# Optimization experiments

Hardware: AMD Instinct MI355X
Metric: run time of the kernel (lower is better)

Reference implementation:

```python
import jax, jax.numpy as jnp
import numpy as np

MODEL_DIM = 2048
NUM_HEADS = 32
HEAD_DIM = 64
NUM_KV_HEADS = 8
ROPE_BASE = 10000.0
BATCH = 2
SEQ = 2048


def setup_inputs() -> dict:
    key = jax.random.key(0)
    ks = jax.random.split(key, 5)
    sd = 1.0 / np.sqrt(MODEL_DIM)
    x = jax.random.normal(ks[0], (BATCH, SEQ, MODEL_DIM), dtype=jnp.float32)
    Wq = jax.random.normal(ks[1], (MODEL_DIM, NUM_HEADS * HEAD_DIM), dtype=jnp.float32) * sd
    Wk = jax.random.normal(ks[2], (MODEL_DIM, NUM_KV_HEADS * HEAD_DIM), dtype=jnp.float32) * sd
    Wv = jax.random.normal(ks[3], (MODEL_DIM, NUM_KV_HEADS * HEAD_DIM), dtype=jnp.float32) * sd
    Wo = jax.random.normal(ks[4], (NUM_HEADS * HEAD_DIM, MODEL_DIM), dtype=jnp.float32) * sd
    return {"x": x, "Wq": Wq, "Wk": Wk, "Wv": Wv, "Wo": Wo}


def _rope_cache(seq_len, head_dim, base, dtype):
    # inv_freq over even dims, standard rotate-half (Llama-style) RoPE cache
    inv_freq = 1.0 / (base ** (jnp.arange(0, head_dim, 2, dtype=jnp.float32) / head_dim))
    t = jnp.arange(seq_len, dtype=jnp.float32)
    freqs = jnp.outer(t, inv_freq)               # [S, hd/2]
    emb = jnp.concatenate([freqs, freqs], axis=-1)  # [S, hd]
    return jnp.cos(emb).astype(dtype), jnp.sin(emb).astype(dtype)


def _rotate_half(x):
    h = x.shape[-1] // 2
    return jnp.concatenate([-x[..., h:], x[..., :h]], axis=-1)


def _apply_rope(q, k, cos, sin):
    # q,k: [B, H, S, hd]; cos,sin: [S, hd] -> broadcast over batch/heads
    cos = cos[None, None, :, :]
    sin = sin[None, None, :, :]
    q = q * cos + _rotate_half(q) * sin
    k = k * cos + _rotate_half(k) * sin
    return q, k


def reference(x, Wq, Wk, Wv, Wo):
    bsz, seq_len, _ = x.shape
    q_per_kv = NUM_HEADS // NUM_KV_HEADS

    # projections -> [B, H, S, hd]
    q = (x @ Wq).reshape(bsz, seq_len, NUM_HEADS, HEAD_DIM).transpose(0, 2, 1, 3)
    k = (x @ Wk).reshape(bsz, seq_len, NUM_KV_HEADS, HEAD_DIM).transpose(0, 2, 1, 3)
    v = (x @ Wv).reshape(bsz, seq_len, NUM_KV_HEADS, HEAD_DIM).transpose(0, 2, 1, 3)

    # GQA: repeat_interleave KV heads to match Q heads
    k = jnp.repeat(k, q_per_kv, axis=1)
    v = jnp.repeat(v, q_per_kv, axis=1)

    cos, sin = _rope_cache(seq_len, HEAD_DIM, ROPE_BASE, x.dtype)
    q, k = _apply_rope(q, k, cos, sin)

    scale = 1.0 / np.sqrt(HEAD_DIM)
    scores = jnp.einsum('bhqd,bhkd->bhqk', q, k) * scale  # [B,H,S,S]
    causal = jnp.tril(jnp.ones((seq_len, seq_len), dtype=bool))
    scores = jnp.where(causal[None, None], scores, jnp.finfo(scores.dtype).min)
    attn = jax.nn.softmax(scores, axis=-1)
    y = jnp.einsum('bhqk,bhkd->bhqd', attn, v)  # [B,H,S,hd]

    y = y.transpose(0, 2, 1, 3).reshape(bsz, seq_len, NUM_HEADS * HEAD_DIM)
    return y @ Wo
```

## Files before the change

### kernel.cpp

```cpp
#include <hip/hip_runtime.h>
#include <cstdint>

typedef unsigned short u16;
typedef __attribute__((ext_vector_type(8))) short short8;
typedef __attribute__((ext_vector_type(4))) short short4v;
typedef __attribute__((ext_vector_type(4))) float f32x4;

#define SEQ     2048
#define NHEADS  32
#define NKV     8
#define HD      64
#define DM      2048
#define MROWS   4096
#define KVSTR   1024
#define PSTR    88

__device__ __forceinline__ float b2f(unsigned int u) {
    return __builtin_bit_cast(float, u << 16);
}
__device__ __forceinline__ u16 f2b(float f) {
    unsigned int u = __builtin_bit_cast(unsigned int, f);
    return (u16)((u + 0x7fffu + ((u >> 16) & 1u)) >> 16);
}
__device__ __forceinline__ unsigned int cvt_pk_bf16(float lo, float hi) {
    unsigned int r;
    asm("v_cvt_pk_bf16_f32 %0, %1, %2" : "=v"(r) : "v"(lo), "v"(hi));
    return r;
}
__device__ __forceinline__ float exp2_raw(float x) {
    return __builtin_amdgcn_exp2f(x);
}

__device__ __forceinline__ float dpp_red_max16(float x) {
    int v = __builtin_bit_cast(int, x);
    x = fmaxf(x, __builtin_bit_cast(float,
        __builtin_amdgcn_update_dpp(v, v, 0xB1, 0xF, 0xF, true)));
    v = __builtin_bit_cast(int, x);
    x = fmaxf(x, __builtin_bit_cast(float,
        __builtin_amdgcn_update_dpp(v, v, 0x4E, 0xF, 0xF, true)));
    v = __builtin_bit_cast(int, x);
    x = fmaxf(x, __builtin_bit_cast(float,
        __builtin_amdgcn_update_dpp(v, v, 0x141, 0xF, 0xF, true)));
    v = __builtin_bit_cast(int, x);
    x = fmaxf(x, __builtin_bit_cast(float,
        __builtin_amdgcn_update_dpp(v, v, 0x140, 0xF, 0xF, true)));
    return x;
}
__device__ __forceinline__ float dpp_red_sum16(float x) {
    int v = __builtin_bit_cast(int, x);
    x = x + __builtin_bit_cast(float,
        __builtin_amdgcn_update_dpp(v, v, 0xB1, 0xF, 0xF, true));
    v = __builtin_bit_cast(int, x);
    x = x + __builtin_bit_cast(float,
        __builtin_amdgcn_update_dpp(v, v, 0x4E, 0xF, 0xF, true));
    v = __builtin_bit_cast(int, x);
    x = x + __builtin_bit_cast(float,
        __builtin_amdgcn_update_dpp(v, v, 0x141, 0xF, 0xF, true));
    v = __builtin_bit_cast(int, x);
    x = x + __builtin_bit_cast(float,
        __builtin_amdgcn_update_dpp(v, v, 0x140, 0xF, 0xF, true));
    return x;
}

#define GLOAD_LDS16(g, l)                                              \
    __builtin_amdgcn_global_load_lds(                                  \
        (const __attribute__((address_space(1))) void*)(g),            \
        (__attribute__((address_space(3))) void*)(l), 16, 0, 0)

__global__ __launch_bounds__(256) void cvt_f32_bf16(
    const float* __restrict__ in, u16* __restrict__ out, int n4) {
    int i = blockIdx.x * 256 + threadIdx.x;
    if (i < n4) {
        float4 v = ((const float4*)in)[i];
        ushort4 o;
        o.x = f2b(v.x); o.y = f2b(v.y); o.z = f2b(v.z); o.w = f2b(v.w);
        ((ushort4*)out)[i] = o;
    }
}

__global__ __launch_bounds__(256) void rope_table_kernel(
    float* __restrict__ cosT, float* __restrict__ sinT) {
    int idx = blockIdx.x * 256 + threadIdx.x;
    int s  = idx >> 5;
    int dl = idx & 31;
    float inv_freq = exp2f((float)dl * -0.41524101186092025f);
    float ang = (float)s * inv_freq;
    float sn, cs;
    sincosf(ang, &sn, &cs);
    cosT[idx] = cs;
    sinT[idx] = sn;
}

__global__ __launch_bounds__(256) void transpose_f32_bf16(
    const float* __restrict__ in, u16* __restrict__ out, int K, int N) {
    __shared__ float tile[32][33];
    int n0 = blockIdx.x * 32, k0 = blockIdx.y * 32;
    int tx = threadIdx.x, ty = threadIdx.y;
    for (int r = ty; r < 32; r += 8)
        tile[r][tx] = in[(size_t)(k0 + r) * N + n0 + tx];
    __syncthreads();
    for (int r = ty; r < 32; r += 8)
        out[(size_t)(n0 + r) * K + k0 + tx] = f2b(tile[tx][r]);
}

#define GEMM_BODY(Aptr, BTptr, Kdim)                                        \
    __shared__ __align__(16) u16 rA[3][4096];                               \
    __shared__ __align__(16) u16 rB[3][4096];                               \
    const int tid  = threadIdx.x;                                           \
    const int wid  = tid >> 6;                                              \
    const int lane = tid & 63;                                              \
    const int quad = lane >> 4;                                             \
    const int l16  = lane & 15;                                             \
    const int nwg  = gridDim.x * gridDim.y;                                 \
    const int fid  = blockIdx.y * gridDim.x + blockIdx.x;                   \
    const int swz  = (fid & 7) * (nwg >> 3) + (fid >> 3);                   \
    const int rowBase = (swz / gridDim.x) * 128;                            \
    const int colBase = (swz % gridDim.x) * 128;                            \
    const int wr = (wid >> 1) * 64;                                         \
    const int wc = (wid & 1) * 64;                                          \
    size_t sAoff[2], sBoff[2];                                              \
    int ldOff[2];                                                           \
    _Pragma("unroll")                                                       \
    for (int j = 0; j < 2; ++j) {                                           \
        const int p = j * 256 + tid;       \
        const int q = p >> 3;                                               \
        const int u = (p & 7) ^ (q & 7);               \
        const int r = (q << 1) | (u >> 2);                                  \
        const int sc = (u & 3) * 8;              \
        sAoff[j] = (size_t)(rowBase + r) * (Kdim) + sc;                     \
        sBoff[j] = (size_t)(colBase + r) * (Kdim) + sc;                     \
        ldOff[j] = (j * 256 + (wid << 6)) * 8;    \
    }                                                                       \
    int aOff[4], bOff[4];                  \
    _Pragma("unroll")                                                       \
    for (int mi = 0; mi < 4; ++mi) {                                        \
        const int ra = wr + mi * 16 + l16;                                  \
        const int qa = ra >> 1;                                             \
        const int ua = ((ra & 1) << 2) | quad;                              \
        aOff[mi] = (qa * 8 + (ua ^ (qa & 7))) * 8;                          \
        const int rb = wc + mi * 16 + l16;                                  \
        const int qb = rb >> 1;                                             \
        const int ub = ((rb & 1) << 2) | quad;                              \
        bOff[mi] = (qb * 8 + (ub ^ (qb & 7))) * 8;                          \
    }                                                                       \
    f32x4 acc[4][4] = {};                                                   \
    const int NT = (Kdim) / 32;                                             \
    _Pragma("unroll")                                                       \
    for (int st = 0; st < 2; ++st) {         \
        _Pragma("unroll")                                                   \
        for (int j = 0; j < 2; ++j) {                                       \
            GLOAD_LDS16(Aptr  + sAoff[j] + st * 32, &rA[st][ldOff[j]]);     \
            GLOAD_LDS16(BTptr + sBoff[j] + st * 32, &rB[st][ldOff[j]]);     \
        }                                                                   \
    }                                                                       \
    int bs = 0;                            \
    for (int s = 0; s < NT; ++s) {                                          \
        if (s < NT - 1)                                                     \
            asm volatile("s_waitcnt vmcnt(4)\n\ts_barrier" ::: "memory");   \
        else                                                                \
            asm volatile("s_waitcnt vmcnt(0)\n\ts_barrier" ::: "memory");   \
        const u16* Ab = rA[bs];                                             \
        const u16* Bb = rB[bs];                                             \
        short8 a[4], b[4];                                                  \
        _Pragma("unroll")                                                   \
        for (int mi = 0; mi < 4; ++mi) a[mi] = *(const short8*)&Ab[aOff[mi]]; \
        _Pragma("unroll")                                                   \
        for (int ni = 0; ni < 4; ++ni) b[ni] = *(const short8*)&Bb[bOff[ni]]; \
        if (s + 2 < NT) {                    \
            const int bi = bs == 0 ? 2 : bs - 1;               \
            const int kk = (s + 2) * 32;                                    \
            _Pragma("unroll")                                               \
            for (int j = 0; j < 2; ++j) {                                   \
                GLOAD_LDS16(Aptr  + sAoff[j] + kk, &rA[bi][ldOff[j]]);      \
                GLOAD_LDS16(BTptr + sBoff[j] + kk, &rB[bi][ldOff[j]]);      \
            }                                                               \
        }                                                                   \
        __builtin_amdgcn_s_setprio(1);                                      \
        _Pragma("unroll")                                                   \
        for (int mi = 0; mi < 4; ++mi)                                      \
            _Pragma("unroll")                                               \
            for (int ni = 0; ni < 4; ++ni)                                  \
                acc[mi][ni] = __builtin_amdgcn_mfma_f32_16x16x32_bf16(      \
                    a[mi], b[ni], acc[mi][ni], 0, 0, 0);                    \
        __builtin_amdgcn_s_setprio(0);                                      \
        bs = bs == 2 ? 0 : bs + 1;                                          \
    }                                                                       \
    const int wRow = rowBase + wr;                                          \
    const int wCol = colBase + wc;

__global__ __launch_bounds__(256, 3) void gemm_qkv(
    const u16* __restrict__ A, const u16* __restrict__ BT,
    u16* __restrict__ Qb, u16* __restrict__ KVb,
    const float* __restrict__ cosT, const float* __restrict__ sinT) {
    GEMM_BODY(A, BT, DM)

    u16* dst;
    int dstride, dcol;
    float scale;
    bool doRope;
    if (wCol < 2048)      { dst = Qb;  dstride = 2048; dcol = wCol;
                            scale = 0.18033688011112042f; doRope = true;  }
    else if (wCol < 2560) { dst = KVb; dstride = 1024; dcol = wCol - 2048; scale = 1.0f; doRope = true;  }
    else                  { dst = KVb; dstride = 1024; dcol = wCol - 2048; scale = 1.0f; doRope = false; }

#pragma unroll
    for (int mi = 0; mi < 4; ++mi) {
#pragma unroll
        for (int r = 0; r < 4; ++r) {
            const int R = wRow + mi * 16 + quad * 4 + r;
            u16* crow = dst + (size_t)R * dstride + dcol;
            if (doRope) {
                const int s = R & (SEQ - 1);
#pragma unroll
                for (int ni = 0; ni < 2; ++ni) {
                    const int dl = ni * 16 + l16;
                    float lo = acc[mi][ni][r];
                    float hi = acc[mi][ni + 2][r];
                    float cs = cosT[s * 32 + dl];
                    float sn = sinT[s * 32 + dl];
                    crow[dl]      = f2b((lo * cs - hi * sn) * scale);
                    crow[dl + 32] = f2b((hi * cs + lo * sn) * scale);
                }
            } else {
#pragma unroll
                for (int ni = 0; ni < 4; ++ni)
                    crow[ni * 16 + l16] = f2b(acc[mi][ni][r]);
            }
        }
    }
}

__global__ __launch_bounds__(256, 3) void gemm_out(
    const u16* __restrict__ A, const u16* __restrict__ BT,
    float* __restrict__ C32) {
    GEMM_BODY(A, BT, DM)
#pragma unroll
    for (int mi = 0; mi < 4; ++mi) {
#pragma unroll
        for (int r = 0; r < 4; ++r) {
            const int R = wRow + mi * 16 + quad * 4 + r;
            float* crow = C32 + (size_t)R * DM + wCol;
#pragma unroll
            for (int ni = 0; ni < 4; ++ni)
                crow[ni * 16 + l16] = acc[mi][ni][r];
        }
    }
}

__global__ __launch_bounds__(256, 3) void flash_attn(
    const u16* __restrict__ Q, const u16* __restrict__ KV,
    u16* __restrict__ Yb, float* __restrict__ PoA,
    float* __restrict__ Ml) {
    __shared__ __align__(16) u16 Ks[64 * 64];
    __shared__ __align__(16) u16 Vt[64 * 72];
    __shared__ __align__(16) u16 Ps[4 * 32 * PSTR];

    const int p   = blockIdx.x >> 1;
    const int sh  = blockIdx.x & 1;
    const int h   = blockIdx.y;
    const int b   = blockIdx.z;
    const int kvh = h >> 2;
    const int tid  = threadIdx.x;
    const int wid  = tid >> 6;
    const int lane = tid & 63;
    const int quad = lane >> 4;
    const int l16  = lane & 15;

    const u16* Kg = KV + (size_t)b * SEQ * KVSTR + kvh * HD;
    const u16* Vg = Kg + 512;
    u16* Psw = Ps + wid * 32 * PSTR;

    const int kKey = tid >> 2;
    const int kC0  = (tid & 3) * 2;
    const int vkp  = tid & 31;
    const int vd0  = (tid >> 5) * 8;

    for (int ph = 0; ph < 2; ++ph) {
        const int qt = ph ? (15 - p) : p;
        const int hc = ph ? (16 - p) : (p + 1);
        const int tS = sh * hc;
        const int rowBaseW = qt * 128 + wid * 32;

        short8 qf[2][2];
#pragma unroll
        for (int rt = 0; rt < 2; ++rt)
#pragma unroll
            for (int ks = 0; ks < 2; ++ks)
                qf[rt][ks] = *(const short8*)&Q[
                    (size_t)(b * SEQ + rowBaseW + rt * 16 + l16) * (NHEADS * HD)
                    + h * HD + ks * 32 + quad * 8];

        f32x4 o[2][4] = {};
        float mi[8], li[8];
#pragma unroll
        for (int i = 0; i < 8; ++i) { mi[i] = -3e38f; li[i] = 0.f; }

        const size_t jF = (size_t)tS * 64;
        short8 kreg0 = *(const short8*)&Kg[(jF + kKey) * KVSTR + kC0 * 8];
        short8 kreg1 = *(const short8*)&Kg[(jF + kKey) * KVSTR + kC0 * 8 + 8];
        short8 vA = *(const short8*)&Vg[(jF + 2 * vkp)     * KVSTR + vd0];
        short8 vB = *(const short8*)&Vg[(jF + 2 * vkp + 1) * KVSTR + vd0];

        for (int tt = 0; tt < hc; ++tt) {
            const int j0 = (tS + tt) * 64;
            __syncthreads();

            *(short8*)&Ks[kKey * 64 + (((kC0)     ^ (kKey & 7)) * 8)] = kreg0;
            *(short8*)&Ks[kKey * 64 + (((kC0 + 1) ^ (kKey & 7)) * 8)] = kreg1;
#pragma unroll
            for (int i = 0; i < 8; ++i) {
                unsigned int w = (unsigned int)(u16)vA[i]
                               | ((unsigned int)(u16)vB[i] << 16);
                ((unsigned int*)Vt)[(vd0 + i) * 36 + vkp] = w;
            }
            __syncthreads();

            if (tt + 1 < hc) {
                const size_t jn = (size_t)(j0 + 64);
                kreg0 = *(const short8*)&Kg[(jn + kKey) * KVSTR + kC0 * 8];
                kreg1 = *(const short8*)&Kg[(jn + kKey) * KVSTR + kC0 * 8 + 8];
                vA = *(const short8*)&Vg[(jn + 2 * vkp)     * KVSTR + vd0];
                vB = *(const short8*)&Vg[(jn + 2 * vkp + 1) * KVSTR + vd0];
            }

            f32x4 s[2][4] = {};
#pragma unroll
            for (int ks = 0; ks < 2; ++ks)
#pragma unroll
                for (int ct = 0; ct < 4; ++ct) {
                    int key = ct * 16 + l16;
                    int cc  = (ks * 4 + quad) ^ (key & 7);
                    short8 bk = *(const short8*)&Ks[key * 64 + cc * 8];
                    s[0][ct] = __builtin_amdgcn_mfma_f32_16x16x32_bf16(
                        qf[0][ks], bk, s[0][ct], 0, 0, 0);
                    s[1][ct] = __builtin_amdgcn_mfma_f32_16x16x32_bf16(
                        qf[1][ks], bk, s[1][ct], 0, 0, 0);
                }

#pragma unroll
            for (int rt = 0; rt < 2; ++rt) {
                const int rB = rowBaseW + rt * 16;
                if (j0 + 63 > rB) {
#pragma unroll
                    for (int ct = 0; ct < 4; ++ct)
#pragma unroll
                        for (int r = 0; r < 4; ++r) {
                            int R = rB + quad * 4 + r;
                            int J = j0 + ct * 16 + l16;
                            if (J > R) s[rt][ct][r] = -3e38f;
                        }
                }
            }

#pragma unroll
            for (int rt = 0; rt < 2; ++rt)
#pragma unroll
                for (int r = 0; r < 4; ++r) {
                    const int ix = rt * 4 + r;
                    float rmax = fmaxf(fmaxf(s[rt][0][r], s[rt][1][r]),
                                       fmaxf(s[rt][2][r], s[rt][3][r]));
                    rmax = dpp_red_max16(rmax);
                    if (!__all(rmax <= mi[ix] + 11.54f)) {
                        float mnew  = fmaxf(mi[ix], rmax);
                        float alpha = exp2_raw(mi[ix] - mnew);
                        mi[ix] = mnew;
                        li[ix] *= alpha;
#pragma unroll
                        for (int ct = 0; ct < 4; ++ct) o[rt][ct][r] *= alpha;
                    }
                    float rs = 0.f;
#pragma unroll
                    for (int ct = 0; ct < 4; ++ct) {
                        float pv = exp2_raw(s[rt][ct][r] - mi[ix]);
                        s[rt][ct][r] = pv;
                        rs += pv;
                    }
                    rs = dpp_red_sum16(rs);
                    li[ix] += rs;
                }

#pragma unroll
            for (int rt = 0; rt < 2; ++rt)
#pragma unroll
                for (int ct = 0; ct < 4; ++ct)
#pragma unroll
                    for (int rp = 0; rp < 2; ++rp) {
                        unsigned int pk = cvt_pk_bf16(s[rt][ct][2 * rp],
                                                      s[rt][ct][2 * rp + 1]);
                        const int row = rt * 16 + quad * 4 + 2 * rp;
                        Psw[row * PSTR + ct * 16 + l16]       = (u16)pk;
                        Psw[(row + 1) * PSTR + ct * 16 + l16] = (u16)(pk >> 16);
                    }

#pragma unroll
            for (int ks = 0; ks < 2; ++ks) {
                short8 pa0 = *(const short8*)&Psw[l16 * PSTR + ks * 32 + quad * 8];
                short8 pa1 = *(const short8*)&Psw[(16 + l16) * PSTR + ks * 32 + quad * 8];
#pragma unroll
                for (int ct = 0; ct < 4; ++ct) {
                    short8 vbf = *(const short8*)&Vt[(ct * 16 + l16) * 72 + ks * 32 + quad * 8];
                    o[0][ct] = __builtin_amdgcn_mfma_f32_16x16x32_bf16(
                        pa0, vbf, o[0][ct], 0, 0, 0);
                    o[1][ct] = __builtin_amdgcn_mfma_f32_16x16x32_bf16(
                        pa1, vbf, o[1][ct], 0, 0, 0);
                }
            }
        }

        float rli[8];
#pragma unroll
        for (int i = 0; i < 8; ++i)
            rli[i] = li[i] > 0.f ? 1.0f / li[i] : 0.f;
        if (sh == 0) {
#pragma unroll
            for (int rt = 0; rt < 2; ++rt)
#pragma unroll
                for (int r = 0; r < 4; ++r) {
                    int R = rowBaseW + rt * 16 + quad * 4 + r;
                    float* arow = PoA + (size_t)(b * SEQ + R) * (NHEADS * HD) + h * HD;
#pragma unroll
                    for (int ct = 0; ct < 4; ++ct)
                        arow[ct * 16 + l16] = o[rt][ct][r] * rli[rt * 4 + r];
                }
        } else {
#pragma unroll
            for (int rt = 0; rt < 2; ++rt)
#pragma unroll
                for (int r = 0; r < 4; ++r) {
                    int R = rowBaseW + rt * 16 + quad * 4 + r;
                    u16* yrow = Yb + (size_t)(b * SEQ + R) * (NHEADS * HD) + h * HD;
#pragma unroll
                    for (int ct = 0; ct < 4; ++ct)
                        yrow[ct * 16 + l16] = f2b(o[rt][ct][r] * rli[rt * 4 + r]);
                }
        }
        if (l16 == 0) {
            float2* MlX = (float2*)Ml + (size_t)sh * 131072
                        + ((b * 32 + h) * 2048 + rowBaseW + quad * 4);
#pragma unroll
            for (int rt = 0; rt < 2; ++rt)
#pragma unroll
                for (int r = 0; r < 4; ++r)
                    MlX[rt * 16 + r] = make_float2(mi[rt * 4 + r], li[rt * 4 + r]);
        }
    }
}

__global__ __launch_bounds__(256) void combine_kernel(
    const float* __restrict__ PoA, const float* __restrict__ Ml,
    u16* __restrict__ Yb) {
    const size_t e = ((size_t)blockIdx.x * 256 + threadIdx.x) * 8;
    const int rowg = (int)(e >> 11);
    const int c    = (int)(e & 2047);
    const int h    = c >> 6;
    const int bz   = rowg >> 11;
    const int row  = rowg & 2047;
    const int slot = ((bz * 32 + h) * 2048 + row) * 2;
    const float mA = Ml[slot],          lA = Ml[slot + 1];
    const float mB = Ml[262144 + slot], lB = Ml[262144 + slot + 1];
    const float m  = fmaxf(mA, mB);
    const float wA = lA * __builtin_amdgcn_exp2f(mA - m);
    const float wB = lB * __builtin_amdgcn_exp2f(mB - m);
    const float inv = 1.0f / (wA + wB);
    const float a = wA * inv, bw = wB * inv;
    float4 A0 = *(const float4*)(PoA + e);
    float4 A1 = *(const float4*)(PoA + e + 4);
    short8 Bv = *(const short8*)(Yb + e);
    float av[8] = {A0.x, A0.y, A0.z, A0.w, A1.x, A1.y, A1.z, A1.w};
    u16 yo[8];
#pragma unroll
    for (int j = 0; j < 8; ++j)
        yo[j] = f2b(a * av[j] + bw * b2f((unsigned int)(u16)Bv[j]));
    *(short8*)(Yb + e) = *(short8*)yo;
}

extern "C" void kernel_launch(void* const* d_in, const int* in_sizes, int n_in,
                              void* d_out, int out_size, void* d_ws, size_t ws_size,
                              hipStream_t stream) {
    const float* x  = (const float*)d_in[0];
    const float* Wq = (const float*)d_in[1];
    const float* Wk = (const float*)d_in[2];
    const float* Wv = (const float*)d_in[3];
    const float* Wo = (const float*)d_in[4];
    float* out = (float*)d_out;

    char* ws = (char*)d_ws;
    u16*  xb    = (u16*)(ws);
    u16*  WqkvT = (u16*)(ws + 16777216);
    u16*  WoT   = (u16*)(ws + 29360128);
    u16*  Qb    = (u16*)(ws + 37748736);
    u16*  KVb   = (u16*)(ws + 54525952);
    u16*  Yb    = (u16*)(ws + 62914560);
    float* cosT = (float*)(ws + 79691776);
    float* sinT = (float*)(ws + 79953920);
    float* PoA  = (float*)(ws);
    float* Ml   = (float*)(ws + 33554432);

    rope_table_kernel<<<dim3(65536 / 256), 256, 0, stream>>>(cosT, sinT);

    cvt_f32_bf16<<<dim3(MROWS * DM / 4 / 256), 256, 0, stream>>>(x, xb, MROWS * DM / 4);

    dim3 tb(32, 8);
    transpose_f32_bf16<<<dim3(2048/32, 2048/32), tb, 0, stream>>>(Wq, WqkvT, 2048, 2048);
    transpose_f32_bf16<<<dim3( 512/32, 2048/32), tb, 0, stream>>>(Wk, WqkvT + 2048 * 2048, 2048, 512);
    transpose_f32_bf16<<<dim3( 512/32, 2048/32), tb, 0, stream>>>(Wv, WqkvT + 2560 * 2048, 2048, 512);

    gemm_qkv<<<dim3(24, 32), 256, 0, stream>>>(xb, WqkvT, Qb, KVb, cosT, sinT);

    flash_attn<<<dim3(16, NHEADS, 2), 256, 0, stream>>>(Qb, KVb, Yb, PoA, Ml);

    combine_kernel<<<dim3(4096), 256, 0, stream>>>(PoA, Ml, Yb);

    transpose_f32_bf16<<<dim3(2048/32, 2048/32), tb, 0, stream>>>(Wo, WoT, 2048, 2048);

    gemm_out<<<dim3(16, 32), 256, 0, stream>>>(Yb, WoT, out);
}
```

Measured before the change: 333.7 us.

## Double-buffer K/V shared tiles in flash attention with one barrier per tile

Splits the K and V shared-memory tiles into two buffers. The next tile is written into the alternate buffer while the current one is consumed, and global loads are issued two tiles ahead. This removes one of the two __syncthreads per key tile. The P staging stride also shrinks from 88 to 72, which keeps LDS usage in check but may change bank-conflict behavior. Total shared memory grows, which could reduce occupancy below the 3 blocks per CU that the launch bounds request.

```diff
diff --git a/kernel.cpp b/kernel.cpp
--- a/kernel.cpp
+++ b/kernel.cpp
@@ -13,7 +13,7 @@
 #define DM      2048
 #define MROWS   4096
 #define KVSTR   1024
-#define PSTR    88
+#define PSTR    72
 
 __device__ __forceinline__ float b2f(unsigned int u) {
     return __builtin_bit_cast(float, u << 16);
@@ -251,8 +251,8 @@
     const u16* __restrict__ Q, const u16* __restrict__ KV,
     u16* __restrict__ Yb, float* __restrict__ PoA,
     float* __restrict__ Ml) {
-    __shared__ __align__(16) u16 Ks[64 * 64];
-    __shared__ __align__(16) u16 Vt[64 * 72];
+    __shared__ __align__(16) u16 Ks[2][64 * 64];
+    __shared__ __align__(16) u16 Vt[2][64 * 72];
     __shared__ __align__(16) u16 Ps[4 * 32 * PSTR];
 
     const int p   = blockIdx.x >> 1;
@@ -295,28 +295,48 @@
 #pragma unroll
         for (int i = 0; i < 8; ++i) { mi[i] = -3e38f; li[i] = 0.f; }
 
-        const size_t jF = (size_t)tS * 64;
-        short8 kreg0 = *(const short8*)&Kg[(jF + kKey) * KVSTR + kC0 * 8];
-        short8 kreg1 = *(const short8*)&Kg[(jF + kKey) * KVSTR + kC0 * 8 + 8];
-        short8 vA = *(const short8*)&Vg[(jF + 2 * vkp)     * KVSTR + vd0];
-        short8 vB = *(const short8*)&Vg[(jF + 2 * vkp + 1) * KVSTR + vd0];
+        {
+            const size_t jF = (size_t)tS * 64;
+            short8 k0 = *(const short8*)&Kg[(jF + kKey) * KVSTR + kC0 * 8];
+            short8 k1 = *(const short8*)&Kg[(jF + kKey) * KVSTR + kC0 * 8 + 8];
+            short8 v0 = *(const short8*)&Vg[(jF + 2 * vkp)     * KVSTR + vd0];
+            short8 v1 = *(const short8*)&Vg[(jF + 2 * vkp + 1) * KVSTR + vd0];
+            *(short8*)&Ks[0][kKey * 64 + (((kC0)     ^ (kKey & 7)) * 8)] = k0;
+            *(short8*)&Ks[0][kKey * 64 + (((kC0 + 1) ^ (kKey & 7)) * 8)] = k1;
+#pragma unroll
+            for (int i = 0; i < 8; ++i) {
+                unsigned int w = (unsigned int)(u16)v0[i]
+                               | ((unsigned int)(u16)v1[i] << 16);
+                ((unsigned int*)Vt[0])[(vd0 + i) * 36 + vkp] = w;
+            }
+        }
+        short8 kreg0, kreg1, vA, vB;
+        if (hc > 1) {
+            const size_t jN = (size_t)(tS + 1) * 64;
+            kreg0 = *(const short8*)&Kg[(jN + kKey) * KVSTR + kC0 * 8];
+            kreg1 = *(const short8*)&Kg[(jN + kKey) * KVSTR + kC0 * 8 + 8];
+            vA = *(const short8*)&Vg[(jN + 2 * vkp)     * KVSTR + vd0];
+            vB = *(const short8*)&Vg[(jN + 2 * vkp + 1) * KVSTR + vd0];
+        }
+        __syncthreads();
 
         for (int tt = 0; tt < hc; ++tt) {
+            const int cur = tt & 1;
             const int j0 = (tS + tt) * 64;
-            __syncthreads();
-
-            *(short8*)&Ks[kKey * 64 + (((kC0)     ^ (kKey & 7)) * 8)] = kreg0;
-            *(short8*)&Ks[kKey * 64 + (((kC0 + 1) ^ (kKey & 7)) * 8)] = kreg1;
-#pragma unroll
-            for (int i = 0; i < 8; ++i) {
-                unsigned int w = (unsigned int)(u16)vA[i]
-                               | ((unsigned int)(u16)vB[i] << 16);
-                ((unsigned int*)Vt)[(vd0 + i) * 36 + vkp] = w;
+
+            if (tt + 1 < hc) {
+                const int nb = cur ^ 1;
+                *(short8*)&Ks[nb][kKey * 64 + (((kC0)     ^ (kKey & 7)) * 8)] = kreg0;
+                *(short8*)&Ks[nb][kKey * 64 + (((kC0 + 1) ^ (kKey & 7)) * 8)] = kreg1;
+#pragma unroll
+                for (int i = 0; i < 8; ++i) {
+                    unsigned int w = (unsigned int)(u16)vA[i]
+                                   | ((unsigned int)(u16)vB[i] << 16);
+                    ((unsigned int*)Vt[nb])[(vd0 + i) * 36 + vkp] = w;
+                }
             }
-            __syncthreads();
-
-            if (tt + 1 < hc) {
-                const size_t jn = (size_t)(j0 + 64);
+            if (tt + 2 < hc) {
+                const size_t jn = (size_t)(j0 + 128);
                 kreg0 = *(const short8*)&Kg[(jn + kKey) * KVSTR + kC0 * 8];
                 kreg1 = *(const short8*)&Kg[(jn + kKey) * KVSTR + kC0 * 8 + 8];
                 vA = *(const short8*)&Vg[(jn + 2 * vkp)     * KVSTR + vd0];
@@ -330,7 +350,7 @@
                 for (int ct = 0; ct < 4; ++ct) {
                     int key = ct * 16 + l16;
                     int cc  = (ks * 4 + quad) ^ (key & 7);
-                    short8 bk = *(const short8*)&Ks[key * 64 + cc * 8];
+                    short8 bk = *(const short8*)&Ks[cur][key * 64 + cc * 8];
                     s[0][ct] = __builtin_amdgcn_mfma_f32_16x16x32_bf16(
                         qf[0][ks], bk, s[0][ct], 0, 0, 0);
                     s[1][ct] = __builtin_amdgcn_mfma_f32_16x16x32_bf16(
@@ -398,13 +418,15 @@
                 short8 pa1 = *(const short8*)&Psw[(16 + l16) * PSTR + ks * 32 + quad * 8];
 #pragma unroll
                 for (int ct = 0; ct < 4; ++ct) {
-                    short8 vbf = *(const short8*)&Vt[(ct * 16 + l16) * 72 + ks * 32 + quad * 8];
+                    short8 vbf = *(const short8*)&Vt[cur][(ct * 16 + l16) * 72 + ks * 32 + quad * 8];
                     o[0][ct] = __builtin_amdgcn_mfma_f32_16x16x32_bf16(
                         pa0, vbf, o[0][ct], 0, 0, 0);
                     o[1][ct] = __builtin_amdgcn_mfma_f32_16x16x32_bf16(
                         pa1, vbf, o[1][ct], 0, 0, 0);
                 }
             }
+
+            __syncthreads();
         }
 
         float rli[8];
```

Result: no change. 335.9 us (+0.6%).
